# Kernel optimization log

Measured on AMD Instinct MI355X. Metric: run time of the kernel, lower is better.

## Reference

```python
import jax, jax.numpy as jnp
import numpy as np

N, S, EMBED, LATENT, HVGS, E = 8192, 128, 256, 128, 2000, 131072


def setup_inputs() -> dict:
    key = jax.random.key(0)
    ks = jax.random.split(key, 12)
    sd = lambda fan_in: 1.0 / np.sqrt(fan_in)
    inp = {
        "emb": jax.random.normal(ks[0], (N, S, EMBED), dtype=jnp.float32),
        "edge_index": jax.random.randint(ks[1], (2, E), 0, N, dtype=jnp.int64),
        "Wq": jax.random.uniform(ks[2], (EMBED, LATENT), jnp.float32, -sd(EMBED), sd(EMBED)),
        "bq": jnp.zeros((LATENT,), jnp.float32),
        "Wk": jax.random.uniform(ks[3], (EMBED, LATENT), jnp.float32, -sd(EMBED), sd(EMBED)),
        "bk": jnp.zeros((LATENT,), jnp.float32),
        "Wv": jax.random.uniform(ks[4], (EMBED, LATENT), jnp.float32, -sd(EMBED), sd(EMBED)),
        "bv": jnp.zeros((LATENT,), jnp.float32),
        "Wo": jax.random.uniform(ks[5], (LATENT, LATENT), jnp.float32, -sd(LATENT), sd(LATENT)),
        "bo": jnp.zeros((LATENT,), jnp.float32),
        "Wg": jax.random.uniform(ks[6], (LATENT, HVGS), jnp.float32, -sd(LATENT), sd(LATENT)),
        "bg": jnp.zeros((HVGS,), jnp.float32),
    }
    return inp


def _gcn(x, W, b, edge_index):
    # PyG GCNConv with add_self_loops=True, symmetric normalization
    h = x @ W  # [N, HVGS]
    n = x.shape[0]
    loop = jnp.arange(n, dtype=edge_index.dtype)
    src = jnp.concatenate([edge_index[0], loop])
    dst = jnp.concatenate([edge_index[1], loop])
    deg = jax.ops.segment_sum(jnp.ones_like(src, dtype=h.dtype), dst, num_segments=n)
    dinv = jnp.where(deg > 0, jax.lax.rsqrt(deg), 0.0)
    norm = dinv[src] * dinv[dst]  # [E+N]
    out = jax.ops.segment_sum(h[src] * norm[:, None], dst, num_segments=n)
    return out + b


def reference(emb, edge_index, Wq, bq, Wk, bk, Wv, bv, Wo, bo, Wg, bg):
    Q = emb @ Wq + bq  # [N, S, L]
    K = emb @ Wk + bk
    V = emb @ Wv + bv
    scale = 1.0 / np.sqrt(emb.shape[-1])
    att_weights = jnp.tanh(jnp.einsum("nsl,ntl->nst", Q, K) * scale)  # [N, S, S]
    att_out = jnp.einsum("nst,ntl->nsl", att_weights, V)
    z = (att_out @ Wo + bo).mean(axis=1)  # [N, L]
    output = _gcn(z, Wg, bg, edge_index)  # [N, HVGS]
    return (att_weights, z, output)
```

## Files before the change

### kernel.cpp

```cpp
#include <hip/hip_runtime.h>
#include <cstdint>
#include <cstddef>

#define NN   8192
#define SS   128
#define EMBD 256
#define LL   128
#define HV   2000
#define EE   131072

typedef float  f32x4  __attribute__((ext_vector_type(4)));
typedef __bf16 bf16x8 __attribute__((ext_vector_type(8)));
typedef unsigned int   u32x4 __attribute__((ext_vector_type(4)));
typedef unsigned short u16x4 __attribute__((ext_vector_type(4)));

__device__ __forceinline__ unsigned short f2bf(float f) {
  unsigned u; __builtin_memcpy(&u, &f, 4);
  unsigned r = u + 0x7fffu + ((u >> 16) & 1u);
  return (unsigned short)(r >> 16);
}

__global__ void prep_w(const float* __restrict__ Wq, const float* __restrict__ Wk,
                       unsigned short* __restrict__ wT) {
  int idx = blockIdx.x * 256 + threadIdx.x;
  int c = idx >> 8, e = idx & 255;
  float v = (c < 128) ? Wq[(size_t)e * LL + c] : Wk[(size_t)e * LL + (c - 128)];
  wT[idx] = f2bf(v);
}

#define QA_LDS (65536 + 4096)
__global__ __launch_bounds__(512, 4)
void qkatt(const float* __restrict__ emb, const unsigned short* __restrict__ wT,
           const float* __restrict__ bq, const float* __restrict__ bk,
           float* __restrict__ attOut, float* __restrict__ cOut)
{
  extern __shared__ char lds[];
  unsigned short* sE = (unsigned short*)lds;
  float* scr = (float*)(lds + 65536);

  const int n    = blockIdx.x;
  const int tid  = threadIdx.x;
  const int wid  = tid >> 6;
  const int lane = tid & 63;
  const int lx   = lane & 15;
  const int g    = lane >> 4;
  const int sw   = (lx & 7) << 3;

  const float* embN = emb + (size_t)n * (SS * EMBD);

  {
    const f32x4* src = (const f32x4*)embN;
    #pragma unroll
    for (int it = 0; it < 16; it++) {
      int i = it * 512 + tid;
      f32x4 v = src[i];
      int s = i >> 6, e0 = (i & 63) << 2;
      u16x4 h;
      h[0] = f2bf(v[0]); h[1] = f2bf(v[1]); h[2] = f2bf(v[2]); h[3] = f2bf(v[3]);
      *(u16x4*)(sE + s * 256 + (e0 ^ ((s & 7) << 3))) = h;
    }
  }
  __syncthreads();

  const int col0 = (wid << 5) + lx;
  float bias[2];
  bias[0] = (col0      < 128) ? bq[col0]      : bk[col0 - 128];
  bias[1] = (col0 + 16 < 128) ? bq[col0 + 16] : bk[col0 + 16 - 128];

  #pragma unroll 1
  for (int half = 0; half < 2; half++) {
    f32x4 acc[2][4];
    #pragma unroll
    for (int n2 = 0; n2 < 2; n2++)
      #pragma unroll
      for (int m = 0; m < 4; m++) acc[n2][m] = f32x4{0.f, 0.f, 0.f, 0.f};

    #pragma unroll
    for (int n2 = 0; n2 < 2; n2++) {
      u32x4 B[8];
      const unsigned short* wp = wT + (size_t)(col0 + n2 * 16) * 256 + g * 8;
      #pragma unroll
      for (int ks = 0; ks < 8; ks++) B[ks] = *(const u32x4*)(wp + ks * 32);
      #pragma unroll
      for (int m = 0; m < 4; m++) {
        const unsigned short* ap = sE + (half * 64 + m * 16 + lx) * 256;
        #pragma unroll
        for (int ks = 0; ks < 8; ks++) {
          u32x4 A = *(const u32x4*)(ap + ((ks * 32 + g * 8) ^ sw));
          acc[n2][m] = __builtin_amdgcn_mfma_f32_16x16x32_bf16(
                         __builtin_bit_cast(bf16x8, A), __builtin_bit_cast(bf16x8, B[ks]),
                         acc[n2][m], 0, 0, 0);
        }
      }
    }
    __syncthreads();

    #pragma unroll
    for (int n2 = 0; n2 < 2; n2++) {
      const int col = col0 + n2 * 16;
      const float bb = bias[n2];
      #pragma unroll
      for (int m = 0; m < 4; m++)
        #pragma unroll
        for (int r = 0; r < 4; r++) {
          const int srow = half * 64 + m * 16 + g * 4 + r;
          sE[srow * 256 + (col ^ ((srow & 7) << 3))] = f2bf(acc[n2][m][r] + bb);
        }
    }
  }
  __syncthreads();

  bf16x8 qf[4];
  #pragma unroll
  for (int ks = 0; ks < 4; ks++)
    qf[ks] = __builtin_bit_cast(bf16x8,
      *(const u32x4*)(sE + (wid * 16 + lx) * 256 + ((ks * 32 + g * 8) ^ sw)));

  f32x4 accS[8];
  #pragma unroll
  for (int nt = 0; nt < 8; nt++) accS[nt] = f32x4{0.f, 0.f, 0.f, 0.f};
  #pragma unroll
  for (int nt = 0; nt < 8; nt++) {
    const int tr = nt * 16 + lx;
    #pragma unroll
    for (int ks = 0; ks < 4; ks++) {
      u32x4 t = *(const u32x4*)(sE + tr * 256 + 128 + ((ks * 32 + g * 8) ^ sw));
      accS[nt] = __builtin_amdgcn_mfma_f32_16x16x32_bf16(
                   qf[ks], __builtin_bit_cast(bf16x8, t), accS[nt], 0, 0, 0);
    }
  }

  {
    float* slot = attOut + (size_t)n * (SS * SS);
    const int srow0 = wid * 16 + g * 4;
    float colp[8];
    #pragma unroll
    for (int nt = 0; nt < 8; nt++) {
      float p = 0.f;
      #pragma unroll
      for (int r = 0; r < 4; r++) {
        float x  = accS[nt][r] * 0.0625f;
        float ax = fabsf(x);
        float ex = __expf(ax * 2.0f);
        float th = __builtin_copysignf(__fdividef(ex - 1.0f, ex + 1.0f), x);
        p += th;
        slot[(size_t)(srow0 + r) * SS + nt * 16 + lx] = th;
      }
      p += __shfl_xor(p, 16, 64);
      p += __shfl_xor(p, 32, 64);
      colp[nt] = p;
    }
    if (lane < 16) {
      #pragma unroll
      for (int nt = 0; nt < 8; nt++) scr[wid * 128 + nt * 16 + lane] = colp[nt];
    }
  }
  __syncthreads();

  if (tid < 128) {
    float s = 0.f;
    #pragma unroll
    for (int w = 0; w < 8; w++) s += scr[w * 128 + tid];
    cOut[(size_t)n * 128 + tid] = s * (1.0f / 128.0f);
  }
}

__global__ __launch_bounds__(256)
void zker(const float* __restrict__ emb, const float* __restrict__ cIn,
          const float* __restrict__ Wv, const float* __restrict__ bv,
          const float* __restrict__ Wo, const float* __restrict__ bo,
          float* __restrict__ zOut)
{
  __shared__ float cS[128], ceS[256], mS[128], scr2[256], csS[2], scrE[1024];
  const int n = blockIdx.x, tid = threadIdx.x;

  if (tid < 128) {
    float c = cIn[(size_t)n * 128 + tid];
    cS[tid] = c;
    float r = c;
    #pragma unroll
    for (int off = 32; off >= 1; off >>= 1) r += __shfl_down(r, off, 64);
    if ((tid & 63) == 0) csS[tid >> 6] = r;
  }
  __syncthreads();

  {
    const int h = tid >> 6, lane = tid & 63;
    const f32x4* e4 = (const f32x4*)(emb + (size_t)n * (SS * EMBD));
    f32x4 acc = f32x4{0.f, 0.f, 0.f, 0.f};
    #pragma unroll 8
    for (int t = h; t < 128; t += 4)
      acc += cS[t] * e4[(size_t)t * 64 + lane];
    *(f32x4*)(scrE + h * 256 + lane * 4) = acc;
  }
  __syncthreads();
  if (tid < 256)
    ceS[tid] = scrE[tid] + scrE[256 + tid] + scrE[512 + tid] + scrE[768 + tid];
  __syncthreads();

  {
    const int l = tid & 127, h = tid >> 7;
    float a = 0.f;
    #pragma unroll 8
    for (int i = 0; i < 128; i++)
      a += ceS[h * 128 + i] * Wv[(size_t)(h * 128 + i) * LL + l];
    scr2[tid] = a;
  }
  __syncthreads();
  if (tid < 128) {
    float csum = csS[0] + csS[1];
    mS[tid] = scr2[tid] + scr2[128 + tid] + csum * bv[tid];
  }
  __syncthreads();

  {
    const int j = tid & 127, h = tid >> 7;
    float a = 0.f;
    #pragma unroll 8
    for (int i = 0; i < 64; i++)
      a += mS[h * 64 + i] * Wo[(size_t)(h * 64 + i) * LL + j];
    scr2[tid] = a;
  }
  __syncthreads();
  if (tid < 128)
    zOut[(size_t)n * LL + tid] = scr2[tid] + scr2[128 + tid] + bo[tid];
}

__global__ void gcn_deg(const int* __restrict__ eidx, float* __restrict__ deg) {
  int e = blockIdx.x * 256 + threadIdx.x;
  if (e < EE) atomicAdd(&deg[eidx[EE + e]], 1.0f);
}

__global__ void gcn_dinv(const float* __restrict__ deg, float* __restrict__ dinv) {
  int i = blockIdx.x * 256 + threadIdx.x;
  if (i < NN) dinv[i] = rsqrtf(deg[i] + 1.0f);
}

__global__ void gcn_self(const float* __restrict__ dinv, const float* __restrict__ z,
                         float* __restrict__ agg) {
  size_t gidx = (size_t)blockIdx.x * 256 + threadIdx.x;
  int i = (int)(gidx >> 7);
  float di = dinv[i];
  agg[gidx] = di * di * z[gidx];
}

__global__ void gcn_scatter(const int* __restrict__ eidx, const float* __restrict__ dinv,
                            const float* __restrict__ z, float* __restrict__ agg) {
  int w    = (blockIdx.x * blockDim.x + threadIdx.x) >> 6;
  int lane = threadIdx.x & 63;
  int nw   = (gridDim.x * blockDim.x) >> 6;
  for (int e = w; e < EE; e += nw) {
    int s = eidx[e], d = eidx[EE + e];
    float nrm = dinv[s] * dinv[d];
    atomicAdd(&agg[(size_t)d * 128 + lane],      nrm * z[(size_t)s * 128 + lane]);
    atomicAdd(&agg[(size_t)d * 128 + 64 + lane], nrm * z[(size_t)s * 128 + 64 + lane]);
  }
}

__global__ __launch_bounds__(256)
void out_gemm(const float* __restrict__ agg, const float* __restrict__ Wg,
              const float* __restrict__ bg, float* __restrict__ outp) {
  __shared__ float sA[8 * 128];
  const int nb = blockIdx.x * 8;
  const int tid = threadIdx.x;
  {
    const float4* src = (const float4*)(agg + (size_t)nb * 128);
    ((float4*)sA)[tid] = src[tid];
  }
  __syncthreads();
  const int g0 = tid * 8;
  if (g0 < HV) {
    float acc[8][8];
    #pragma unroll
    for (int i = 0; i < 8; i++)
      #pragma unroll
      for (int j = 0; j < 8; j++) acc[i][j] = 0.0f;
    #pragma unroll 2
    for (int l = 0; l < 128; l++) {
      float4 wa = *(const float4*)(Wg + (size_t)l * HV + g0);
      float4 wb = *(const float4*)(Wg + (size_t)l * HV + g0 + 4);
      float w[8] = {wa.x, wa.y, wa.z, wa.w, wb.x, wb.y, wb.z, wb.w};
      #pragma unroll
      for (int i = 0; i < 8; i++) {
        float a = sA[i * 128 + l];
        #pragma unroll
        for (int j = 0; j < 8; j++) acc[i][j] += a * w[j];
      }
    }
    float b[8];
    #pragma unroll
    for (int j = 0; j < 8; j++) b[j] = bg[g0 + j];
    #pragma unroll
    for (int i = 0; i < 8; i++) {
      float4 oa = make_float4(acc[i][0] + b[0], acc[i][1] + b[1], acc[i][2] + b[2], acc[i][3] + b[3]);
      float4 ob = make_float4(acc[i][4] + b[4], acc[i][5] + b[5], acc[i][6] + b[6], acc[i][7] + b[7]);
      *(float4*)(outp + (size_t)(nb + i) * HV + g0)     = oa;
      *(float4*)(outp + (size_t)(nb + i) * HV + g0 + 4) = ob;
    }
  }
}

extern "C" void kernel_launch(void* const* d_in, const int* in_sizes, int n_in,
                              void* d_out, int out_size, void* d_ws, size_t ws_size,
                              hipStream_t stream) {
  const float* emb  = (const float*)d_in[0];
  const int*   eidx = (const int*)d_in[1];
  const float* Wq = (const float*)d_in[2];
  const float* bq = (const float*)d_in[3];
  const float* Wk = (const float*)d_in[4];
  const float* bk = (const float*)d_in[5];
  const float* Wv = (const float*)d_in[6];
  const float* bv = (const float*)d_in[7];
  const float* Wo = (const float*)d_in[8];
  const float* bo = (const float*)d_in[9];
  const float* Wg = (const float*)d_in[10];
  const float* bg = (const float*)d_in[11];

  float* out  = (float*)d_out;
  float* attO = out;
  float* zO   = out + (size_t)NN * SS * SS;
  float* oO   = zO + (size_t)NN * LL;

  float* wsf  = (float*)d_ws;
  float* deg  = wsf;
  float* dinv = wsf + NN;
  float* agg  = wsf + 2 * NN;
  unsigned short* wT = (unsigned short*)(wsf + 2 * NN + (size_t)NN * 128);
  float* cWS  = wsf + 2 * NN + (size_t)NN * 128 + 32768;

  (void)in_sizes; (void)n_in; (void)out_size; (void)ws_size;

  hipFuncSetAttribute((const void*)qkatt,
                      hipFuncAttributeMaxDynamicSharedMemorySize, QA_LDS);

  hipMemsetAsync(deg, 0, NN * sizeof(float), stream);
  gcn_deg <<<EE / 256, 256, 0, stream>>>(eidx, deg);
  gcn_dinv<<<NN / 256, 256, 0, stream>>>(deg, dinv);
  prep_w  <<<(2 * LL * EMBD) / 256, 256, 0, stream>>>(Wq, Wk, wT);

  qkatt<<<NN, 512, QA_LDS, stream>>>(emb, wT, bq, bk, attO, cWS);
  zker <<<NN, 256, 0, stream>>>(emb, cWS, Wv, bv, Wo, bo, zO);

  gcn_self   <<<NN * 128 / 256, 256, 0, stream>>>(dinv, zO, agg);
  gcn_scatter<<<2048, 256, 0, stream>>>(eidx, dinv, zO, agg);
  out_gemm   <<<NN / 8, 256, 0, stream>>>(agg, Wg, bg, oO);
}
```

Before: 850.4 us.

## Fuse V projection and z computation into the attention kernel

Computes V = emb·Wv on MFMA inside qkatt, reusing the bf16 emb tile already staged in LDS, then forms m = cᵀV and z = m·Wo + bo in the same block. This removes the separate zker kernel, which re-read all of emb from global memory (about 1 GB), and drops the c round-trip through the workspace. In exchange qkatt holds 32 extra accumulator registers per lane, which may cut occupancy under launch_bounds(512,4). V is now computed in bf16 instead of fp32, so precision drops slightly.

```diff
diff --git a/kernel.cpp b/kernel.cpp
--- a/kernel.cpp
+++ b/kernel.cpp
@@ -21,22 +21,30 @@
 }
 
 __global__ void prep_w(const float* __restrict__ Wq, const float* __restrict__ Wk,
-                       unsigned short* __restrict__ wT) {
+                       const float* __restrict__ Wv, unsigned short* __restrict__ wT) {
   int idx = blockIdx.x * 256 + threadIdx.x;
   int c = idx >> 8, e = idx & 255;
-  float v = (c < 128) ? Wq[(size_t)e * LL + c] : Wk[(size_t)e * LL + (c - 128)];
+  float v = (c < 128) ? Wq[(size_t)e * LL + c]
+          : (c < 256) ? Wk[(size_t)e * LL + (c - 128)]
+                      : Wv[(size_t)e * LL + (c - 256)];
   wT[idx] = f2bf(v);
 }
 
-#define QA_LDS (65536 + 4096)
+#define QA_LDS 73728
 __global__ __launch_bounds__(512, 4)
 void qkatt(const float* __restrict__ emb, const unsigned short* __restrict__ wT,
            const float* __restrict__ bq, const float* __restrict__ bk,
-           float* __restrict__ attOut, float* __restrict__ cOut)
+           const float* __restrict__ bv,
+           const float* __restrict__ Wo, const float* __restrict__ bo,
+           float* __restrict__ attOut, float* __restrict__ zOut)
 {
   extern __shared__ char lds[];
   unsigned short* sE = (unsigned short*)lds;
-  float* scr = (float*)(lds + 65536);
+  float* scr  = (float*)(lds + 65536);
+  float* cL   = (float*)(lds + 69632);
+  float* mS   = (float*)(lds + 70144);
+  float* scrZ = (float*)(lds + 70656);
+  float* csS  = (float*)(lds + 72704);
 
   const int n    = blockIdx.x;
   const int tid  = threadIdx.x;
@@ -63,9 +71,14 @@
   __syncthreads();
 
   const int col0 = (wid << 5) + lx;
+  const int vcol = (wid << 4) + lx;
   float bias[2];
   bias[0] = (col0      < 128) ? bq[col0]      : bk[col0 - 128];
   bias[1] = (col0 + 16 < 128) ? bq[col0 + 16] : bk[col0 + 16 - 128];
+
+  f32x4 accV[8];
+  #pragma unroll
+  for (int j = 0; j < 8; j++) accV[j] = f32x4{0.f, 0.f, 0.f, 0.f};
 
   #pragma unroll 1
   for (int half = 0; half < 2; half++) {
@@ -90,6 +103,23 @@
           acc[n2][m] = __builtin_amdgcn_mfma_f32_16x16x32_bf16(
                          __builtin_bit_cast(bf16x8, A), __builtin_bit_cast(bf16x8, B[ks]),
                          acc[n2][m], 0, 0, 0);
+        }
+      }
+    }
+    {
+      u32x4 B[8];
+      const unsigned short* wp = wT + (size_t)(256 + vcol) * 256 + g * 8;
+      #pragma unroll
+      for (int ks = 0; ks < 8; ks++) B[ks] = *(const u32x4*)(wp + ks * 32);
+      #pragma unroll
+      for (int m = 0; m < 4; m++) {
+        const unsigned short* ap = sE + (half * 64 + m * 16 + lx) * 256;
+        #pragma unroll
+        for (int ks = 0; ks < 8; ks++) {
+          u32x4 A = *(const u32x4*)(ap + ((ks * 32 + g * 8) ^ sw));
+          accV[half * 4 + m] = __builtin_amdgcn_mfma_f32_16x16x32_bf16(
+                         __builtin_bit_cast(bf16x8, A), __builtin_bit_cast(bf16x8, B[ks]),
+                         accV[half * 4 + m], 0, 0, 0);
         }
       }
     }
@@ -161,22 +191,8 @@
     float s = 0.f;
     #pragma unroll
     for (int w = 0; w < 8; w++) s += scr[w * 128 + tid];
-    cOut[(size_t)n * 128 + tid] = s * (1.0f / 128.0f);
-  }
-}
-
-__global__ __launch_bounds__(256)
-void zker(const float* __restrict__ emb, const float* __restrict__ cIn,
-          const float* __restrict__ Wv, const float* __restrict__ bv,
-          const float* __restrict__ Wo, const float* __restrict__ bo,
-          float* __restrict__ zOut)
-{
-  __shared__ float cS[128], ceS[256], mS[128], scr2[256], csS[2], scrE[1024];
-  const int n = blockIdx.x, tid = threadIdx.x;
-
-  if (tid < 128) {
-    float c = cIn[(size_t)n * 128 + tid];
-    cS[tid] = c;
+    float c = s * (1.0f / 128.0f);
+    cL[tid] = c;
     float r = c;
     #pragma unroll
     for (int off = 32; off >= 1; off >>= 1) r += __shfl_down(r, off, 64);
@@ -185,31 +201,19 @@
   __syncthreads();
 
   {
-    const int h = tid >> 6, lane = tid & 63;
-    const f32x4* e4 = (const f32x4*)(emb + (size_t)n * (SS * EMBD));
-    f32x4 acc = f32x4{0.f, 0.f, 0.f, 0.f};
-    #pragma unroll 8
-    for (int t = h; t < 128; t += 4)
-      acc += cS[t] * e4[(size_t)t * 64 + lane];
-    *(f32x4*)(scrE + h * 256 + lane * 4) = acc;
-  }
-  __syncthreads();
-  if (tid < 256)
-    ceS[tid] = scrE[tid] + scrE[256 + tid] + scrE[512 + tid] + scrE[768 + tid];
-  __syncthreads();
-
-  {
-    const int l = tid & 127, h = tid >> 7;
-    float a = 0.f;
-    #pragma unroll 8
-    for (int i = 0; i < 128; i++)
-      a += ceS[h * 128 + i] * Wv[(size_t)(h * 128 + i) * LL + l];
-    scr2[tid] = a;
-  }
-  __syncthreads();
-  if (tid < 128) {
-    float csum = csS[0] + csS[1];
-    mS[tid] = scr2[tid] + scr2[128 + tid] + csum * bv[tid];
+    float p = 0.f;
+    #pragma unroll
+    for (int j = 0; j < 8; j++) {
+      const int rb = (j >> 2) * 64 + (j & 3) * 16 + g * 4;
+      #pragma unroll
+      for (int r = 0; r < 4; r++) p += cL[rb + r] * accV[j][r];
+    }
+    p += __shfl_xor(p, 16, 64);
+    p += __shfl_xor(p, 32, 64);
+    if (lane < 16) {
+      float csum = csS[0] + csS[1];
+      mS[vcol] = p + csum * bv[vcol];
+    }
   }
   __syncthreads();
 
@@ -217,13 +221,14 @@
     const int j = tid & 127, h = tid >> 7;
     float a = 0.f;
     #pragma unroll 8
-    for (int i = 0; i < 64; i++)
-      a += mS[h * 64 + i] * Wo[(size_t)(h * 64 + i) * LL + j];
-    scr2[tid] = a;
+    for (int i = 0; i < 32; i++)
+      a += mS[h * 32 + i] * Wo[(size_t)(h * 32 + i) * LL + j];
+    scrZ[h * 128 + j] = a;
   }
   __syncthreads();
   if (tid < 128)
-    zOut[(size_t)n * LL + tid] = scr2[tid] + scr2[128 + tid] + bo[tid];
+    zOut[(size_t)n * LL + tid] = scrZ[tid] + scrZ[128 + tid] + scrZ[256 + tid]
+                               + scrZ[384 + tid] + bo[tid];
 }
 
 __global__ void gcn_deg(const int* __restrict__ eidx, float* __restrict__ deg) {
@@ -326,7 +331,6 @@
   float* dinv = wsf + NN;
   float* agg  = wsf + 2 * NN;
   unsigned short* wT = (unsigned short*)(wsf + 2 * NN + (size_t)NN * 128);
-  float* cWS  = wsf + 2 * NN + (size_t)NN * 128 + 32768;
 
   (void)in_sizes; (void)n_in; (void)out_size; (void)ws_size;
 
@@ -336,10 +340,9 @@
   hipMemsetAsync(deg, 0, NN * sizeof(float), stream);
   gcn_deg <<<EE / 256, 256, 0, stream>>>(eidx, deg);
   gcn_dinv<<<NN / 256, 256, 0, stream>>>(deg, dinv);
-  prep_w  <<<(2 * LL * EMBD) / 256, 256, 0, stream>>>(Wq, Wk, wT);
-
-  qkatt<<<NN, 512, QA_LDS, stream>>>(emb, wT, bq, bk, attO, cWS);
-  zker <<<NN, 256, 0, stream>>>(emb, cWS, Wv, bv, Wo, bo, zO);
+  prep_w  <<<(3 * LL * EMBD) / 256, 256, 0, stream>>>(Wq, Wk, Wv, wT);
+
+  qkatt<<<NN, 512, QA_LDS, stream>>>(emb, wT, bq, bk, bv, Wo, bo, attO, zO);
 
   gcn_self   <<<NN * 128 / 256, 256, 0, stream>>>(dinv, zO, agg);
   gcn_scatter<<<2048, 256, 0, stream>>>(eidx, dinv, zO, agg);
```

Result: slower. 1.429 ms (+68.1%).

## Compute V projection inside qkatt with MFMA and simplify z kernel

Applied to the files above, without the earlier changes.

The V projection now runs on MFMA inside the QK attention kernel while emb is already resident in LDS. Its bf16 result goes to a workspace buffer, and a new zkerV reads that instead of re-reading fp32 emb. This removes a second full pass over emb (8192x128x256 floats) in the z kernel. In exchange it writes and reads a 256MB-smaller bf16 V tensor, raises LDS per block, adds register pressure in qkatt, and depends on the workspace being large enough. Otherwise it falls back to the old path.

```diff
diff --git a/kernel.cpp b/kernel.cpp
--- a/kernel.cpp
+++ b/kernel.cpp
@@ -19,23 +19,30 @@
   unsigned r = u + 0x7fffu + ((u >> 16) & 1u);
   return (unsigned short)(r >> 16);
 }
+__device__ __forceinline__ float bf2f(unsigned short h) {
+  unsigned x = (unsigned)h << 16; float f; __builtin_memcpy(&f, &x, 4); return f;
+}
 
 __global__ void prep_w(const float* __restrict__ Wq, const float* __restrict__ Wk,
-                       unsigned short* __restrict__ wT) {
+                       const float* __restrict__ Wv, unsigned short* __restrict__ wT) {
   int idx = blockIdx.x * 256 + threadIdx.x;
   int c = idx >> 8, e = idx & 255;
-  float v = (c < 128) ? Wq[(size_t)e * LL + c] : Wk[(size_t)e * LL + (c - 128)];
+  float v = (c < 128) ? Wq[(size_t)e * LL + c]
+          : (c < 256) ? Wk[(size_t)e * LL + (c - 128)]
+                      : Wv[(size_t)e * LL + (c - 256)];
   wT[idx] = f2bf(v);
 }
 
-#define QA_LDS (65536 + 4096)
+#define QA_LDS 81920
 __global__ __launch_bounds__(512, 4)
 void qkatt(const float* __restrict__ emb, const unsigned short* __restrict__ wT,
            const float* __restrict__ bq, const float* __restrict__ bk,
-           float* __restrict__ attOut, float* __restrict__ cOut)
+           float* __restrict__ attOut, float* __restrict__ cOut,
+           unsigned short* __restrict__ Vout)
 {
   extern __shared__ char lds[];
-  unsigned short* sE = (unsigned short*)lds;
+  unsigned short* sE   = (unsigned short*)lds;
+  unsigned short* auxV = (unsigned short*)(lds + 65536);
   float* scr = (float*)(lds + 65536);
 
   const int n    = blockIdx.x;
@@ -63,6 +70,7 @@
   __syncthreads();
 
   const int col0 = (wid << 5) + lx;
+  const int vcol = (wid << 4) + lx;
   float bias[2];
   bias[0] = (col0      < 128) ? bq[col0]      : bk[col0 - 128];
   bias[1] = (col0 + 16 < 128) ? bq[col0 + 16] : bk[col0 + 16 - 128];
@@ -93,6 +101,27 @@
         }
       }
     }
+
+    f32x4 accV[4];
+    if (Vout) {
+      #pragma unroll
+      for (int m = 0; m < 4; m++) accV[m] = f32x4{0.f, 0.f, 0.f, 0.f};
+      u32x4 B[8];
+      const unsigned short* wp = wT + (size_t)(256 + vcol) * 256 + g * 8;
+      #pragma unroll
+      for (int ks = 0; ks < 8; ks++) B[ks] = *(const u32x4*)(wp + ks * 32);
+      #pragma unroll
+      for (int m = 0; m < 4; m++) {
+        const unsigned short* ap = sE + (half * 64 + m * 16 + lx) * 256;
+        #pragma unroll
+        for (int ks = 0; ks < 8; ks++) {
+          u32x4 A = *(const u32x4*)(ap + ((ks * 32 + g * 8) ^ sw));
+          accV[m] = __builtin_amdgcn_mfma_f32_16x16x32_bf16(
+                      __builtin_bit_cast(bf16x8, A), __builtin_bit_cast(bf16x8, B[ks]),
+                      accV[m], 0, 0, 0);
+        }
+      }
+    }
     __syncthreads();
 
     #pragma unroll
@@ -106,6 +135,18 @@
           const int srow = half * 64 + m * 16 + g * 4 + r;
           sE[srow * 256 + (col ^ ((srow & 7) << 3))] = f2bf(acc[n2][m][r] + bb);
         }
+    }
+    if (Vout) {
+      #pragma unroll
+      for (int m = 0; m < 4; m++)
+        #pragma unroll
+        for (int r = 0; r < 4; r++)
+          auxV[(m * 16 + g * 4 + r) * 128 + vcol] = f2bf(accV[m][r]);
+      __syncthreads();
+      const u32x4* s4 = (const u32x4*)auxV;
+      u32x4* dst = (u32x4*)(Vout + ((size_t)n * 128 + half * 64) * 128);
+      dst[tid]       = s4[tid];
+      dst[512 + tid] = s4[512 + tid];
     }
   }
   __syncthreads();
@@ -166,10 +207,58 @@
 }
 
 __global__ __launch_bounds__(256)
-void zker(const float* __restrict__ emb, const float* __restrict__ cIn,
-          const float* __restrict__ Wv, const float* __restrict__ bv,
-          const float* __restrict__ Wo, const float* __restrict__ bo,
-          float* __restrict__ zOut)
+void zkerV(const unsigned short* __restrict__ V, const float* __restrict__ cIn,
+           const float* __restrict__ bv,
+           const float* __restrict__ Wo, const float* __restrict__ bo,
+           float* __restrict__ zOut)
+{
+  __shared__ float cS[128], mS[128], scr2[256], csS[2];
+  const int n = blockIdx.x, tid = threadIdx.x;
+
+  if (tid < 128) {
+    float c = cIn[(size_t)n * 128 + tid];
+    cS[tid] = c;
+    float r = c;
+    #pragma unroll
+    for (int off = 32; off >= 1; off >>= 1) r += __shfl_down(r, off, 64);
+    if ((tid & 63) == 0) csS[tid >> 6] = r;
+  }
+  __syncthreads();
+
+  {
+    const int l = tid & 127, h = tid >> 7;
+    const unsigned short* vp = V + (size_t)n * (128 * 128) + l;
+    float a = 0.f;
+    #pragma unroll 8
+    for (int t = h; t < 128; t += 2)
+      a += cS[t] * bf2f(vp[(size_t)t * 128]);
+    scr2[tid] = a;
+  }
+  __syncthreads();
+  if (tid < 128) {
+    float csum = csS[0] + csS[1];
+    mS[tid] = scr2[tid] + scr2[128 + tid] + csum * bv[tid];
+  }
+  __syncthreads();
+
+  {
+    const int j = tid & 127, h = tid >> 7;
+    float a = 0.f;
+    #pragma unroll 8
+    for (int i = 0; i < 64; i++)
+      a += mS[h * 64 + i] * Wo[(size_t)(h * 64 + i) * LL + j];
+    scr2[tid] = a;
+  }
+  __syncthreads();
+  if (tid < 128)
+    zOut[(size_t)n * LL + tid] = scr2[tid] + scr2[128 + tid] + bo[tid];
+}
+
+__global__ __launch_bounds__(256)
+void zkerE(const float* __restrict__ emb, const float* __restrict__ cIn,
+           const float* __restrict__ Wv, const float* __restrict__ bv,
+           const float* __restrict__ Wo, const float* __restrict__ bo,
+           float* __restrict__ zOut)
 {
   __shared__ float cS[128], ceS[256], mS[128], scr2[256], csS[2], scrE[1024];
   const int n = blockIdx.x, tid = threadIdx.x;
@@ -326,9 +415,15 @@
   float* dinv = wsf + NN;
   float* agg  = wsf + 2 * NN;
   unsigned short* wT = (unsigned short*)(wsf + 2 * NN + (size_t)NN * 128);
-  float* cWS  = wsf + 2 * NN + (size_t)NN * 128 + 32768;
-
-  (void)in_sizes; (void)n_in; (void)out_size; (void)ws_size;
+  float* cWS  = (float*)((char*)wT + 3 * LL * EMBD * sizeof(unsigned short));
+  unsigned short* Vws = (unsigned short*)(cWS + (size_t)NN * 128);
+
+  const size_t needBytes = ((size_t)(2 * NN) + (size_t)NN * 128 + (size_t)NN * 128) * 4
+                         + (size_t)(3 * LL * EMBD) * 2
+                         + (size_t)NN * 128 * 128 * 2;
+  const bool useV = (ws_size >= needBytes);
+
+  (void)in_sizes; (void)n_in; (void)out_size;
 
   hipFuncSetAttribute((const void*)qkatt,
                       hipFuncAttributeMaxDynamicSharedMemorySize, QA_LDS);
@@ -336,10 +431,15 @@
   hipMemsetAsync(deg, 0, NN * sizeof(float), stream);
   gcn_deg <<<EE / 256, 256, 0, stream>>>(eidx, deg);
   gcn_dinv<<<NN / 256, 256, 0, stream>>>(deg, dinv);
-  prep_w  <<<(2 * LL * EMBD) / 256, 256, 0, stream>>>(Wq, Wk, wT);
-
-  qkatt<<<NN, 512, QA_LDS, stream>>>(emb, wT, bq, bk, attO, cWS);
-  zker <<<NN, 256, 0, stream>>>(emb, cWS, Wv, bv, Wo, bo, zO);
+  prep_w  <<<(3 * LL * EMBD) / 256, 256, 0, stream>>>(Wq, Wk, Wv, wT);
+
+  qkatt<<<NN, 512, QA_LDS, stream>>>(emb, wT, bq, bk, attO, cWS,
+                                     useV ? Vws : (unsigned short*)nullptr);
+
+  if (useV)
+    zkerV<<<NN, 256, 0, stream>>>(Vws, cWS, bv, Wo, bo, zO);
+  else
+    zkerE<<<NN, 256, 0, stream>>>(emb, cWS, Wv, bv, Wo, bo, zO);
 
   gcn_self   <<<NN * 128 / 256, 256, 0, stream>>>(dinv, zO, agg);
   gcn_scatter<<<2048, 256, 0, stream>>>(eidx, dinv, zO, agg);
```

New measurement: 3.370 ms. 296% more time.
